# Performance work log

Measured on AMD Instinct MI355X. Metric: run time of the kernel, lower is better.

Reference implementation:

```python
import jax, jax.numpy as jnp
import numpy as np

B, N, D_IN, D = 4, 256, 128, 256
T = 3
EPS = 1e-5


def _layernorm(x, g, b):
    mu = x.mean(axis=-1, keepdims=True)
    var = x.var(axis=-1, keepdims=True)
    return (x - mu) * jax.lax.rsqrt(var + EPS) * g + b


def setup_inputs() -> dict:
    key = jax.random.key(0)
    ks = jax.random.split(key, 16)
    s = lambda k, shape, fan_in: jax.random.normal(k, shape, jnp.float32) / np.sqrt(fan_in)
    return {
        "inputs": jax.random.normal(ks[0], (B, N, D_IN), jnp.float32),
        "v_t": jax.random.normal(ks[1], (B, N, D), jnp.float32),
        "i_t": jnp.zeros((B, N, N), jnp.float32),
        # proj_inputs
        "Wp": s(ks[2], (D_IN, D), D_IN), "bp": jnp.zeros((D,), jnp.float32),
        # MLPAdjacency
        "Wx": s(ks[3], (D, D), D), "bx": jnp.zeros((D,), jnp.float32),
        "wi": s(ks[4], (D,), 1), "bi": jnp.zeros((D,), jnp.float32),
        "ws": s(ks[5], (D,), D), "bs": jnp.zeros((1,), jnp.float32),
        # LayerNorms
        "g_pre": jnp.ones((3 * D,), jnp.float32), "be_pre": jnp.zeros((3 * D,), jnp.float32),
        "g_n": jnp.ones((D,), jnp.float32), "be_n": jnp.zeros((D,), jnp.float32),
        # DeepSet(3D -> D -> D), equivariant layers: h@Wg + mean(h)@Wl + b
        "W1g": s(ks[6], (3 * D, D), 3 * D), "W1l": s(ks[7], (3 * D, D), 3 * D),
        "b1": jnp.zeros((D,), jnp.float32),
        "W2g": s(ks[8], (D, D), D), "W2l": s(ks[9], (D, D), D),
        "b2": jnp.zeros((D,), jnp.float32),
    }


def reference(inputs, v_t, i_t, Wp, bp, Wx, bx, wi, bi, ws, bs,
              g_pre, be_pre, g_n, be_n, W1g, W1l, b1, W2g, W2l, b2):
    x_in = inputs @ Wp + bp  # [b,n,d]
    n_t, inc = v_t, i_t
    preds = []
    for _ in range(T):
        # MLPAdjacency: [b,n,n,d] broadcast sum -> relu -> linear -> sigmoid
        xp = n_t @ Wx + bx
        s = jax.nn.relu(xp[:, None, :, :] + xp[:, :, None, :]
                        + inc[..., None] * wi + bi)
        inc = jax.nn.sigmoid(jnp.einsum('bend,d->ben', s, ws) + bs[0])  # [b,n,n]
        # aggregation
        upd = jnp.einsum('ben,bed->bnd', inc, n_t)
        # DeepSet over normalized concat, residual + LayerNorm
        h = _layernorm(jnp.concatenate([x_in, n_t, upd], axis=-1), g_pre, be_pre)
        m = h.mean(axis=1, keepdims=True)
        h1 = jax.nn.relu(h @ W1g + m @ W1l + b1)
        m1 = h1.mean(axis=1, keepdims=True)
        h2 = h1 @ W2g + m1 @ W2l + b2
        n_t = _layernorm(n_t + h2, g_n, be_n)
        preds.append(inc)
    return (jnp.stack(preds, axis=0), n_t, inc)
```

## Files before the change

kernel.cpp:

```cpp
#include <hip/hip_runtime.h>
#include <cstddef>

#define LN_EPS 1e-5f

__device__ inline float4 ld4(const float* p) { return *reinterpret_cast<const float4*>(p); }
__device__ inline void st4(float* p, float4 v) { *reinterpret_cast<float4*>(p) = v; }

__device__ __forceinline__ void gemm_dev(float* lds, const float* __restrict__ A,
                                         const float* __restrict__ W,
                                         const float* __restrict__ bias,
                                         float* __restrict__ dst,
                                         int K, int chunk, int row0, int col0, int k0) {
  float* At = lds;
  float* Ws = lds + 1088;
  const int tid = threadIdx.x;
  const int tx = tid & 15, ty = tid >> 4;
  float acc[4][4] = {{0.f}};
  const int arow = tid >> 2;
  const int ak4 = (tid & 3) * 4;
  const int wk = tid >> 4;
  const int wc4 = (tid & 15) * 4;
  float4 av = ld4(&A[(size_t)(row0 + arow) * K + k0 + ak4]);
  float4 wv = ld4(&W[(size_t)(k0 + wk) * 256 + col0 + wc4]);
  for (int ks = 0; ks < chunk; ks += 16) {
    __syncthreads();
    At[(ak4 + 0) * 68 + arow] = av.x;
    At[(ak4 + 1) * 68 + arow] = av.y;
    At[(ak4 + 2) * 68 + arow] = av.z;
    At[(ak4 + 3) * 68 + arow] = av.w;
    st4(&Ws[wk * 68 + wc4], wv);
    __syncthreads();
    if (ks + 16 < chunk) {
      av = ld4(&A[(size_t)(row0 + arow) * K + k0 + ks + 16 + ak4]);
      wv = ld4(&W[(size_t)(k0 + ks + 16 + wk) * 256 + col0 + wc4]);
    }
#pragma unroll
    for (int kk = 0; kk < 16; ++kk) {
      float4 a = ld4(&At[kk * 68 + ty * 4]);
      float4 w = ld4(&Ws[kk * 68 + tx * 4]);
      acc[0][0] = fmaf(a.x, w.x, acc[0][0]); acc[0][1] = fmaf(a.x, w.y, acc[0][1]);
      acc[0][2] = fmaf(a.x, w.z, acc[0][2]); acc[0][3] = fmaf(a.x, w.w, acc[0][3]);
      acc[1][0] = fmaf(a.y, w.x, acc[1][0]); acc[1][1] = fmaf(a.y, w.y, acc[1][1]);
      acc[1][2] = fmaf(a.y, w.z, acc[1][2]); acc[1][3] = fmaf(a.y, w.w, acc[1][3]);
      acc[2][0] = fmaf(a.z, w.x, acc[2][0]); acc[2][1] = fmaf(a.z, w.y, acc[2][1]);
      acc[2][2] = fmaf(a.z, w.z, acc[2][2]); acc[2][3] = fmaf(a.z, w.w, acc[2][3]);
      acc[3][0] = fmaf(a.w, w.x, acc[3][0]); acc[3][1] = fmaf(a.w, w.y, acc[3][1]);
      acc[3][2] = fmaf(a.w, w.z, acc[3][2]); acc[3][3] = fmaf(a.w, w.w, acc[3][3]);
    }
  }
  if (bias) {
    float4 b4 = ld4(&bias[col0 + tx * 4]);
#pragma unroll
    for (int i = 0; i < 4; ++i) {
      float4 o;
      o.x = acc[i][0] + b4.x; o.y = acc[i][1] + b4.y;
      o.z = acc[i][2] + b4.z; o.w = acc[i][3] + b4.w;
      st4(&dst[(size_t)(row0 + ty * 4 + i) * 256 + col0 + tx * 4], o);
    }
  } else {
#pragma unroll
    for (int i = 0; i < 4; ++i) {
      float4 o = {acc[i][0], acc[i][1], acc[i][2], acc[i][3]};
      st4(&dst[(size_t)(row0 + ty * 4 + i) * 256 + col0 + tx * 4], o);
    }
  }
}

__device__ __forceinline__ void gemm_h1(float* lds, const float* __restrict__ part,
                                        const float* __restrict__ mt1p,
                                        const float* __restrict__ W,
                                        float* __restrict__ dst,
                                        int gb, int row0, int col0, int k0) {
  float* At = lds;
  float* Ws = lds + 1088;
  float* mt1s = lds + 2176;
  const int tid = threadIdx.x;
  const int tx = tid & 15, ty = tid >> 4;
  if (tid < 64) {
    float s = 0.f;
#pragma unroll
    for (int k2 = 0; k2 < 12; ++k2) s += mt1p[((size_t)(k2 * 4 + gb) << 8) + k0 + tid];
    mt1s[tid] = s;
  }
  float acc[4][4] = {{0.f}};
  const int arow = tid >> 2;
  const int ak4 = (tid & 3) * 4;
  const int wk = tid >> 4;
  const int wc4 = (tid & 15) * 4;
  size_t ao = (size_t)(row0 + arow) * 256 + k0 + ak4;
  float4 p0 = ld4(&part[ao]);
  float4 p1 = ld4(&part[ao + 262144]);
  float4 p2 = ld4(&part[ao + 524288]);
  float4 p3 = ld4(&part[ao + 786432]);
  float4 wv = ld4(&W[(size_t)(k0 + wk) * 256 + col0 + wc4]);
  for (int ks = 0; ks < 64; ks += 16) {
    __syncthreads();
    float4 m = ld4(&mt1s[ks + ak4]);
    float4 av;
    av.x = fmaxf(p0.x + p1.x + p2.x + p3.x + m.x, 0.f);
    av.y = fmaxf(p0.y + p1.y + p2.y + p3.y + m.y, 0.f);
    av.z = fmaxf(p0.z + p1.z + p2.z + p3.z + m.z, 0.f);
    av.w = fmaxf(p0.w + p1.w + p2.w + p3.w + m.w, 0.f);
    At[(ak4 + 0) * 68 + arow] = av.x;
    At[(ak4 + 1) * 68 + arow] = av.y;
    At[(ak4 + 2) * 68 + arow] = av.z;
    At[(ak4 + 3) * 68 + arow] = av.w;
    st4(&Ws[wk * 68 + wc4], wv);
    __syncthreads();
    if (ks + 16 < 64) {
      size_t an = (size_t)(row0 + arow) * 256 + k0 + ks + 16 + ak4;
      p0 = ld4(&part[an]);
      p1 = ld4(&part[an + 262144]);
      p2 = ld4(&part[an + 524288]);
      p3 = ld4(&part[an + 786432]);
      wv = ld4(&W[(size_t)(k0 + ks + 16 + wk) * 256 + col0 + wc4]);
    }
#pragma unroll
    for (int kk = 0; kk < 16; ++kk) {
      float4 a = ld4(&At[kk * 68 + ty * 4]);
      float4 w = ld4(&Ws[kk * 68 + tx * 4]);
      acc[0][0] = fmaf(a.x, w.x, acc[0][0]); acc[0][1] = fmaf(a.x, w.y, acc[0][1]);
      acc[0][2] = fmaf(a.x, w.z, acc[0][2]); acc[0][3] = fmaf(a.x, w.w, acc[0][3]);
      acc[1][0] = fmaf(a.y, w.x, acc[1][0]); acc[1][1] = fmaf(a.y, w.y, acc[1][1]);
      acc[1][2] = fmaf(a.y, w.z, acc[1][2]); acc[1][3] = fmaf(a.y, w.w, acc[1][3]);
      acc[2][0] = fmaf(a.z, w.x, acc[2][0]); acc[2][1] = fmaf(a.z, w.y, acc[2][1]);
      acc[2][2] = fmaf(a.z, w.z, acc[2][2]); acc[2][3] = fmaf(a.z, w.w, acc[2][3]);
      acc[3][0] = fmaf(a.w, w.x, acc[3][0]); acc[3][1] = fmaf(a.w, w.y, acc[3][1]);
      acc[3][2] = fmaf(a.w, w.z, acc[3][2]); acc[3][3] = fmaf(a.w, w.w, acc[3][3]);
    }
  }
#pragma unroll
  for (int i = 0; i < 4; ++i) {
    float4 o = {acc[i][0], acc[i][1], acc[i][2], acc[i][3]};
    st4(&dst[(size_t)(row0 + ty * 4 + i) * 256 + col0 + tx * 4], o);
  }
}

__device__ __forceinline__ void gemmt_dev(float* lds, const float* __restrict__ pred,
                                          const float* __restrict__ nt,
                                          float* __restrict__ pp,
                                          int gb, int n0, int col0, int k0) {
  float* At = lds;
  float* Ws = lds + 1088;
  const int tid = threadIdx.x;
  const int tx = tid & 15, ty = tid >> 4;
  const float* Ab = pred + ((size_t)gb << 16);
  const float* Bb = nt + ((size_t)gb << 16);
  float acc[4][4] = {{0.f}};
  const int ee = tid >> 4;
  const int q4 = (tid & 15) * 4;
  float4 av = ld4(&Ab[((size_t)(k0 + ee) << 8) + n0 + q4]);
  float4 wv = ld4(&Bb[((size_t)(k0 + ee) << 8) + col0 + q4]);
  for (int ks = 0; ks < 64; ks += 16) {
    __syncthreads();
    st4(&At[ee * 68 + q4], av);
    st4(&Ws[ee * 68 + q4], wv);
    __syncthreads();
    if (ks + 16 < 64) {
      av = ld4(&Ab[((size_t)(k0 + ks + 16 + ee) << 8) + n0 + q4]);
      wv = ld4(&Bb[((size_t)(k0 + ks + 16 + ee) << 8) + col0 + q4]);
    }
#pragma unroll
    for (int kk = 0; kk < 16; ++kk) {
      float4 a = ld4(&At[kk * 68 + ty * 4]);
      float4 w = ld4(&Ws[kk * 68 + tx * 4]);
      acc[0][0] = fmaf(a.x, w.x, acc[0][0]); acc[0][1] = fmaf(a.x, w.y, acc[0][1]);
      acc[0][2] = fmaf(a.x, w.z, acc[0][2]); acc[0][3] = fmaf(a.x, w.w, acc[0][3]);
      acc[1][0] = fmaf(a.y, w.x, acc[1][0]); acc[1][1] = fmaf(a.y, w.y, acc[1][1]);
      acc[1][2] = fmaf(a.y, w.z, acc[1][2]); acc[1][3] = fmaf(a.y, w.w, acc[1][3]);
      acc[2][0] = fmaf(a.z, w.x, acc[2][0]); acc[2][1] = fmaf(a.z, w.y, acc[2][1]);
      acc[2][2] = fmaf(a.z, w.z, acc[2][2]); acc[2][3] = fmaf(a.z, w.w, acc[2][3]);
      acc[3][0] = fmaf(a.w, w.x, acc[3][0]); acc[3][1] = fmaf(a.w, w.y, acc[3][1]);
      acc[3][2] = fmaf(a.w, w.z, acc[3][2]); acc[3][3] = fmaf(a.w, w.w, acc[3][3]);
    }
  }
#pragma unroll
  for (int i = 0; i < 4; ++i) {
    float4 o = {acc[i][0], acc[i][1], acc[i][2], acc[i][3]};
    st4(&pp[(((size_t)gb << 8) + n0 + ty * 4 + i) * 256 + col0 + tx * 4], o);
  }
}

__device__ __forceinline__ void wred2(float& s, float& q) {
#pragma unroll
  for (int off = 32; off; off >>= 1) {
    s += __shfl_xor(s, off);
    q += __shfl_xor(q, off);
  }
}

__device__ __forceinline__ void mtk_dev(float* lds, const float* __restrict__ X,
                                        const float* __restrict__ Wl,
                                        const float* __restrict__ bias,
                                        float* __restrict__ mtp, int gb, int ks, int Kd) {
  float* sm = lds;
  float* m64 = lds + 256;
  const int tid = threadIdx.x;
  const int col = tid & 63, q = tid >> 6;
  const float* xb = X + (size_t)(gb * 256 + q * 64) * Kd + ks * 64 + col;
  float s = 0.f;
#pragma unroll 8
  for (int r = 0; r < 64; ++r) s += xb[(size_t)r * Kd];
  sm[tid] = s;
  __syncthreads();
  if (tid < 64) m64[tid] = (sm[tid] + sm[tid + 64] + sm[tid + 128] + sm[tid + 192]) * (1.f / 256.f);
  __syncthreads();
  const int c = tid;
  float acc = (ks == 0) ? bias[c] : 0.f;
  const float* wp = Wl + (size_t)ks * 64 * 256 + c;
#pragma unroll 8
  for (int k = 0; k < 64; ++k) acc = fmaf(m64[k], wp[(size_t)k * 256], acc);
  mtp[((size_t)(ks * 4 + gb) << 8) + c] = acc;
}

__device__ __forceinline__ void mtk_h1(float* lds, const float* __restrict__ part,
                                       const float* __restrict__ mt1p,
                                       const float* __restrict__ Wl,
                                       const float* __restrict__ bias,
                                       float* __restrict__ mtp, int gb, int ks) {
  float* sm = lds;
  float* m64 = lds + 256;
  const int tid = threadIdx.x;
  const int col = tid & 63, q = tid >> 6;
  float mt1v = 0.f;
#pragma unroll
  for (int k2 = 0; k2 < 12; ++k2) mt1v += mt1p[((size_t)(k2 * 4 + gb) << 8) + ks * 64 + col];
  const float* pb = part + (size_t)(gb * 256 + q * 64) * 256 + ks * 64 + col;
  float s = 0.f;
#pragma unroll 4
  for (int r = 0; r < 64; ++r) {
    size_t o = (size_t)r * 256;
    float v = pb[o] + pb[o + 262144] + pb[o + 524288] + pb[o + 786432] + mt1v;
    s += fmaxf(v, 0.f);
  }
  sm[tid] = s;
  __syncthreads();
  if (tid < 64) m64[tid] = (sm[tid] + sm[tid + 64] + sm[tid + 128] + sm[tid + 192]) * (1.f / 256.f);
  __syncthreads();
  const int c = tid;
  float acc = (ks == 0) ? bias[c] : 0.f;
  const float* wp = Wl + (size_t)ks * 64 * 256 + c;
#pragma unroll 8
  for (int k = 0; k < 64; ++k) acc = fmaf(m64[k], wp[(size_t)k * 256], acc);
  mtp[((size_t)(ks * 4 + gb) << 8) + c] = acc;
}


__global__ __launch_bounds__(256) void k_gemm(const float* __restrict__ A,
                                              const float* __restrict__ W,
                                              const float* __restrict__ bias,
                                              float* __restrict__ dst,
                                              int K, int chunk) {
  __shared__ float lds[2176];
  float* base = bias ? dst : dst + (size_t)blockIdx.z * 262144;
  gemm_dev(lds, A, W, bias, base, K, chunk,
           blockIdx.x * 64, blockIdx.y * 64, blockIdx.z * chunk);
}

__global__ __launch_bounds__(256) void k_gemm0(const float* __restrict__ v_t,
                                               const float* __restrict__ Wx,
                                               float* __restrict__ part,
                                               const float* __restrict__ inputs,
                                               const float* __restrict__ Wp,
                                               const float* __restrict__ bp,
                                               float* __restrict__ x_in) {
  __shared__ float lds[2176];
  const int b = blockIdx.x;
  if (b < 256) {
    int mt = b & 15, ntile = (b >> 4) & 3, kz = b >> 6;
    gemm_dev(lds, v_t, Wx, nullptr, part + (size_t)kz * 262144, 256, 64,
             mt * 64, ntile * 64, kz * 64);
  } else {
    int idx = b - 256;
    int mt = idx & 15, ntile = idx >> 4;
    gemm_dev(lds, inputs, Wp, bp, x_in, 128, 128, mt * 64, ntile * 64, 0);
  }
}

__global__ __launch_bounds__(256) void k_adj(const float* __restrict__ part,
                                             const float* __restrict__ incold,
                                             const float* __restrict__ wi,
                                             const float* __restrict__ bi,
                                             const float* __restrict__ bx,
                                             const float* __restrict__ wsv,
                                             const float* __restrict__ bs,
                                             float* __restrict__ pred,
                                             float* __restrict__ pred2) {
  __shared__ float lds[8448];
  float* tn = lds;
  float* te = lds + 32 * 132;
  const int n0 = blockIdx.x * 32, e0 = blockIdx.y * 32, gb = blockIdx.z;
  const int tid = threadIdx.x;
  const size_t rb = (size_t)gb * 256;
  const int tx = tid & 15, ty = tid >> 4;
  float incv[2][2], acc[2][2];
#pragma unroll
  for (int j = 0; j < 2; ++j)
#pragma unroll
    for (int i = 0; i < 2; ++i) {
      incv[j][i] = incold[((rb + e0 + ty + 16 * j) << 8) + n0 + tx + 16 * i];
      acc[j][i] = 0.f;
    }
  for (int dh = 0; dh < 256; dh += 128) {
    if (dh) __syncthreads();
#pragma unroll
    for (int s = 0; s < 4; ++s) {
      int idx = tid + s * 256;
      int row = idx >> 5;
      int d = dh + (idx & 31) * 4;
      float4 bxv = ld4(&bx[d]);
      {
        size_t o = ((rb + n0 + row) << 8) + d;
        float4 p0 = ld4(&part[o]);
        float4 p1 = ld4(&part[o + 262144]);
        float4 p2 = ld4(&part[o + 524288]);
        float4 p3 = ld4(&part[o + 786432]);
        float4 v;
        v.x = p0.x + p1.x + p2.x + p3.x + bxv.x;
        v.y = p0.y + p1.y + p2.y + p3.y + bxv.y;
        v.z = p0.z + p1.z + p2.z + p3.z + bxv.z;
        v.w = p0.w + p1.w + p2.w + p3.w + bxv.w;
        st4(&tn[row * 132 + (d - dh)], v);
      }
      {
        size_t o = ((rb + e0 + row) << 8) + d;
        float4 p0 = ld4(&part[o]);
        float4 p1 = ld4(&part[o + 262144]);
        float4 p2 = ld4(&part[o + 524288]);
        float4 p3 = ld4(&part[o + 786432]);
        float4 bv = ld4(&bi[d]);
        float4 v;
        v.x = p0.x + p1.x + p2.x + p3.x + bxv.x + bv.x;
        v.y = p0.y + p1.y + p2.y + p3.y + bxv.y + bv.y;
        v.z = p0.z + p1.z + p2.z + p3.z + bxv.z + bv.z;
        v.w = p0.w + p1.w + p2.w + p3.w + bxv.w + bv.w;
        st4(&te[row * 132 + (d - dh)], v);
      }
    }
    __syncthreads();
#pragma unroll 4
    for (int dl = 0; dl < 128; dl += 4) {
      float4 wiq = ld4(&wi[dh + dl]);
      float4 wsq = ld4(&wsv[dh + dl]);
      float4 xn0 = ld4(&tn[tx * 132 + dl]);
      float4 xn1 = ld4(&tn[(tx + 16) * 132 + dl]);
      float4 xe0 = ld4(&te[ty * 132 + dl]);
      float4 xe1 = ld4(&te[(ty + 16) * 132 + dl]);
#pragma unroll
      for (int j = 0; j < 2; ++j) {
        float4 xe = j ? xe1 : xe0;
#pragma unroll
        for (int i = 0; i < 2; ++i) {
          float4 xn = i ? xn1 : xn0;
          float u;
          u = fmaf(incv[j][i], wiq.x, xn.x + xe.x); u = fmaxf(u, 0.f); acc[j][i] = fmaf(u, wsq.x, acc[j][i]);
          u = fmaf(incv[j][i], wiq.y, xn.y + xe.y); u = fmaxf(u, 0.f); acc[j][i] = fmaf(u, wsq.y, acc[j][i]);
          u = fmaf(incv[j][i], wiq.z, xn.z + xe.z); u = fmaxf(u, 0.f); acc[j][i] = fmaf(u, wsq.z, acc[j][i]);
          u = fmaf(incv[j][i], wiq.w, xn.w + xe.w); u = fmaxf(u, 0.f); acc[j][i] = fmaf(u, wsq.w, acc[j][i]);
        }
      }
    }
  }
  const float b0 = bs[0];
#pragma unroll
  for (int j = 0; j < 2; ++j)
#pragma unroll
    for (int i = 0; i < 2; ++i) {
      float s = acc[j][i] + b0;
      float v = 1.f / (1.f + __expf(-s));
      size_t o = ((rb + e0 + ty + 16 * j) << 8) + n0 + tx + 16 * i;
      pred[o] = v;
      if (pred2) pred2[o] = v;
    }
}

__global__ __launch_bounds__(256) void k_gemmt(const float* __restrict__ pred,
                                               const float* __restrict__ nt,
                                               float* __restrict__ part) {
  __shared__ float lds[2176];
  const int gb = blockIdx.z >> 2, kc = blockIdx.z & 3;
  gemmt_dev(lds, pred, nt, part + (size_t)kc * 262144,
            gb, blockIdx.x * 64, blockIdx.y * 64, kc * 64);
}

__global__ __launch_bounds__(256) void k_ln768(const float* __restrict__ part,
                                               const float* __restrict__ x_in,
                                               const float* __restrict__ nt,
                                               const float* __restrict__ g,
                                               const float* __restrict__ be,
                                               float* __restrict__ h) {
  const int row = blockIdx.x * 4 + (threadIdx.x >> 6);
  const int lane = threadIdx.x & 63;
  const int c4 = lane * 4;
  const size_t ro = (size_t)row * 256 + c4;
  float4 u = ld4(&part[ro]);
  float4 u1 = ld4(&part[ro + 262144]);
  float4 u2 = ld4(&part[ro + 524288]);
  float4 u3 = ld4(&part[ro + 786432]);
  u.x += u1.x + u2.x + u3.x;
  u.y += u1.y + u2.y + u3.y;
  u.z += u1.z + u2.z + u3.z;
  u.w += u1.w + u2.w + u3.w;
  float4 xi = ld4(&x_in[ro]);
  float4 nv = ld4(&nt[ro]);
  float s = xi.x + xi.y + xi.z + xi.w + nv.x + nv.y + nv.z + nv.w + u.x + u.y + u.z + u.w;
  float sq = xi.x * xi.x + xi.y * xi.y + xi.z * xi.z + xi.w * xi.w
           + nv.x * nv.x + nv.y * nv.y + nv.z * nv.z + nv.w * nv.w
           + u.x * u.x + u.y * u.y + u.z * u.z + u.w * u.w;
  wred2(s, sq);
  float mu = s * (1.f / 768.f);
  float rs = rsqrtf(sq * (1.f / 768.f) - mu * mu + LN_EPS);
  float* hr = h + (size_t)row * 768;
  {
    float4 g4 = ld4(&g[c4]), b4 = ld4(&be[c4]), o;
    o.x = (xi.x - mu) * rs * g4.x + b4.x;
    o.y = (xi.y - mu) * rs * g4.y + b4.y;
    o.z = (xi.z - mu) * rs * g4.z + b4.z;
    o.w = (xi.w - mu) * rs * g4.w + b4.w;
    st4(&hr[c4], o);
  }
  {
    float4 g4 = ld4(&g[256 + c4]), b4 = ld4(&be[256 + c4]), o;
    o.x = (nv.x - mu) * rs * g4.x + b4.x;
    o.y = (nv.y - mu) * rs * g4.y + b4.y;
    o.z = (nv.z - mu) * rs * g4.z + b4.z;
    o.w = (nv.w - mu) * rs * g4.w + b4.w;
    st4(&hr[256 + c4], o);
  }
  {
    float4 g4 = ld4(&g[512 + c4]), b4 = ld4(&be[512 + c4]), o;
    o.x = (u.x - mu) * rs * g4.x + b4.x;
    o.y = (u.y - mu) * rs * g4.y + b4.y;
    o.z = (u.z - mu) * rs * g4.z + b4.z;
    o.w = (u.w - mu) * rs * g4.w + b4.w;
    st4(&hr[512 + c4], o);
  }
}

__global__ __launch_bounds__(256) void k_g768mtk(const float* __restrict__ h,
                                                 const float* __restrict__ W1g,
                                                 const float* __restrict__ W1l,
                                                 const float* __restrict__ b1,
                                                 float* __restrict__ part,
                                                 float* __restrict__ mt1p) {
  __shared__ float lds[2176];
  const int b = blockIdx.x;
  if (b < 256) {
    int mt = b & 15, ntile = (b >> 4) & 3, kz = b >> 6;
    gemm_dev(lds, h, W1g, nullptr, part + (size_t)kz * 262144, 768, 192,
             mt * 64, ntile * 64, kz * 192);
  } else {
    int idx = b - 256;
    mtk_dev(lds, h, W1l, b1, mt1p, idx & 3, idx >> 2, 768);
  }
}

__global__ __launch_bounds__(256) void k_gh1mtk2(const float* __restrict__ part,
                                                 const float* __restrict__ mt1p,
                                                 const float* __restrict__ W2g,
                                                 const float* __restrict__ W2l,
                                                 const float* __restrict__ b2,
                                                 float* __restrict__ part2,
                                                 float* __restrict__ mt2p) {
  __shared__ float lds[2240];
  const int b = blockIdx.x;
  if (b < 256) {
    int mt = b & 15, ntile = (b >> 4) & 3, kz = b >> 6;
    gemm_h1(lds, part, mt1p, W2g, part2 + (size_t)kz * 262144,
            mt >> 2, mt * 64, ntile * 64, kz * 64);
  } else {
    int idx = b - 256;
    mtk_h1(lds, part, mt1p, W2l, b2, mt2p, idx & 3, idx >> 2);
  }
}

__global__ __launch_bounds__(256) void k_ln256(const float* __restrict__ part2,
                                               const float* __restrict__ nt,
                                               const float* __restrict__ mt2p,
                                               const float* __restrict__ g,
                                               const float* __restrict__ be,
                                               float* __restrict__ dst) {
  const int row = blockIdx.x * 4 + (threadIdx.x >> 6);
  const int lane = threadIdx.x & 63;
  const int c4 = lane * 4;
  const int gb = row >> 8;
  const size_t ro = (size_t)row * 256 + c4;
  float4 p0 = ld4(&part2[ro]);
  float4 p1 = ld4(&part2[ro + 262144]);
  float4 p2 = ld4(&part2[ro + 524288]);
  float4 p3 = ld4(&part2[ro + 786432]);
  float4 m4 = {0.f, 0.f, 0.f, 0.f};
#pragma unroll
  for (int k2 = 0; k2 < 4; ++k2) {
    float4 mv = ld4(&mt2p[((size_t)(k2 * 4 + gb) << 8) + c4]);
    m4.x += mv.x; m4.y += mv.y; m4.z += mv.z; m4.w += mv.w;
  }
  float4 nv = ld4(&nt[ro]);
  float4 x;
  x.x = nv.x + p0.x + p1.x + p2.x + p3.x + m4.x;
  x.y = nv.y + p0.y + p1.y + p2.y + p3.y + m4.y;
  x.z = nv.z + p0.z + p1.z + p2.z + p3.z + m4.z;
  x.w = nv.w + p0.w + p1.w + p2.w + p3.w + m4.w;
  float s = x.x + x.y + x.z + x.w;
  float sq = x.x * x.x + x.y * x.y + x.z * x.z + x.w * x.w;
  wred2(s, sq);
  float mu = s * (1.f / 256.f);
  float rs = rsqrtf(sq * (1.f / 256.f) - mu * mu + LN_EPS);
  float4 g4 = ld4(&g[c4]), b4 = ld4(&be[c4]), o;
  o.x = (x.x - mu) * rs * g4.x + b4.x;
  o.y = (x.y - mu) * rs * g4.y + b4.y;
  o.z = (x.z - mu) * rs * g4.z + b4.z;
  o.w = (x.w - mu) * rs * g4.w + b4.w;
  st4(&dst[ro], o);
}

extern "C" void kernel_launch(void* const* d_in, const int* in_sizes, int n_in,
                              void* d_out, int out_size, void* d_ws, size_t ws_size,
                              hipStream_t stream) {
  (void)in_sizes; (void)n_in; (void)out_size; (void)ws_size;
  const float* inputs = (const float*)d_in[0];
  const float* v_t    = (const float*)d_in[1];
  const float* i_t    = (const float*)d_in[2];
  const float* Wp     = (const float*)d_in[3];
  const float* bp     = (const float*)d_in[4];
  const float* Wx     = (const float*)d_in[5];
  const float* bx     = (const float*)d_in[6];
  const float* wi     = (const float*)d_in[7];
  const float* bi     = (const float*)d_in[8];
  const float* ws     = (const float*)d_in[9];
  const float* bs     = (const float*)d_in[10];
  const float* g_pre  = (const float*)d_in[11];
  const float* be_pre = (const float*)d_in[12];
  const float* g_n    = (const float*)d_in[13];
  const float* be_n   = (const float*)d_in[14];
  const float* W1g    = (const float*)d_in[15];
  const float* W1l    = (const float*)d_in[16];
  const float* b1     = (const float*)d_in[17];
  const float* W2g    = (const float*)d_in[18];
  const float* W2l    = (const float*)d_in[19];
  const float* b2     = (const float*)d_in[20];
  float* out = (float*)d_out;
  float* wsf = (float*)d_ws;
  float* x_in  = wsf;
  float* ntA   = wsf + 262144;
  float* ntB   = wsf + 524288;
  float* h     = wsf + 786432;
  float* part2 = wsf + 786432;
  float* part  = wsf + 1835008;
  float* mt1p  = wsf + 2883584;
  float* mt2p  = wsf + 2895872;

  for (int t = 0; t < 3; ++t) {
    const float* ntCur = (t == 0) ? v_t : ((t == 1) ? ntA : ntB);
    float* dstNt = (t == 2) ? (out + 786432) : ((t == 0) ? ntA : ntB);
    const float* incold = (t == 0) ? i_t : (out + (size_t)(t - 1) * 262144);
    float* pred = out + (size_t)t * 262144;
    float* pred2 = (t == 2) ? (out + 1048576) : nullptr;

    if (t == 0) {
      k_gemm0<<<320, 256, 0, stream>>>(v_t, Wx, part, inputs, Wp, bp, x_in);
    } else {
      k_gemm<<<dim3(16, 4, 4), 256, 0, stream>>>(ntCur, Wx, nullptr, part, 256, 64);
    }
    k_adj<<<dim3(8, 8, 4), 256, 0, stream>>>(part, incold, wi, bi, bx, ws, bs, pred, pred2);
    k_gemmt<<<dim3(4, 4, 16), 256, 0, stream>>>(pred, ntCur, part);
    k_ln768<<<256, 256, 0, stream>>>(part, x_in, ntCur, g_pre, be_pre, h);
    k_g768mtk<<<304, 256, 0, stream>>>(h, W1g, W1l, b1, part, mt1p);
    k_gh1mtk2<<<272, 256, 0, stream>>>(part, mt1p, W2g, W2l, b2, part2, mt2p);
    k_ln256<<<256, 256, 0, stream>>>(part2, ntCur, mt2p, g_n, be_n, dstNt);
  }
}
```

Baseline: 198.6 us.

## Switch tiled SIMT GEMMs to packed fp16 dot2 with fp32 accumulation

New measurement: 193.4 us (median of 2 runs). 2.6% less time.

```diff
diff --git a/kernel.cpp b/kernel.cpp
--- a/kernel.cpp
+++ b/kernel.cpp
@@ -6,46 +6,73 @@
 __device__ inline float4 ld4(const float* p) { return *reinterpret_cast<const float4*>(p); }
 __device__ inline void st4(float* p, float4 v) { *reinterpret_cast<float4*>(p) = v; }
 
-__device__ __forceinline__ void gemm_dev(float* lds, const float* __restrict__ A,
-                                         const float* __restrict__ W,
-                                         const float* __restrict__ bias,
-                                         float* __restrict__ dst,
-                                         int K, int chunk, int row0, int col0, int k0) {
-  float* At = lds;
-  float* Ws = lds + 1088;
+typedef _Float16 h2_t __attribute__((ext_vector_type(2)));
+
+__device__ __forceinline__ unsigned pack2(float x, float y) {
+  h2_t h;
+  h.x = (_Float16)x;
+  h.y = (_Float16)y;
+  return __builtin_bit_cast(unsigned, h);
+}
+
+__device__ __forceinline__ float dot2(unsigned a, unsigned b, float c) {
+  h2_t ah = __builtin_bit_cast(h2_t, a);
+  h2_t bh = __builtin_bit_cast(h2_t, b);
+#if __has_builtin(__builtin_amdgcn_fdot2)
+  return __builtin_amdgcn_fdot2(ah, bh, c, false);
+#else
+  return fmaf((float)ah.x, (float)bh.x, fmaf((float)ah.y, (float)bh.y, c));
+#endif
+}
+
+__device__ __forceinline__ void gemm16(unsigned* ldsU, const float* __restrict__ A,
+                                       const float* __restrict__ W,
+                                       const float* __restrict__ bias,
+                                       float* __restrict__ dst,
+                                       int K, int chunk, int row0, int col0, int k0) {
+  unsigned* AtU = ldsU;
+  unsigned* WsU = ldsU + 544;
   const int tid = threadIdx.x;
   const int tx = tid & 15, ty = tid >> 4;
+  const int arow = tid >> 2, ak4 = (tid & 3) * 4;
+  const int wkk2 = tid >> 4, wc4 = (tid & 15) * 4;
   float acc[4][4] = {{0.f}};
-  const int arow = tid >> 2;
-  const int ak4 = (tid & 3) * 4;
-  const int wk = tid >> 4;
-  const int wc4 = (tid & 15) * 4;
   float4 av = ld4(&A[(size_t)(row0 + arow) * K + k0 + ak4]);
-  float4 wv = ld4(&W[(size_t)(k0 + wk) * 256 + col0 + wc4]);
+  float4 w0, w1;
+  if (tid < 128) {
+    w0 = ld4(&W[(size_t)(k0 + 2 * wkk2) * 256 + col0 + wc4]);
+    w1 = ld4(&W[(size_t)(k0 + 2 * wkk2 + 1) * 256 + col0 + wc4]);
+  }
   for (int ks = 0; ks < chunk; ks += 16) {
     __syncthreads();
-    At[(ak4 + 0) * 68 + arow] = av.x;
-    At[(ak4 + 1) * 68 + arow] = av.y;
-    At[(ak4 + 2) * 68 + arow] = av.z;
-    At[(ak4 + 3) * 68 + arow] = av.w;
-    st4(&Ws[wk * 68 + wc4], wv);
+    AtU[(ak4 >> 1) * 68 + arow] = pack2(av.x, av.y);
+    AtU[((ak4 >> 1) + 1) * 68 + arow] = pack2(av.z, av.w);
+    if (tid < 128) {
+      WsU[wkk2 * 68 + wc4 + 0] = pack2(w0.x, w1.x);
+      WsU[wkk2 * 68 + wc4 + 1] = pack2(w0.y, w1.y);
+      WsU[wkk2 * 68 + wc4 + 2] = pack2(w0.z, w1.z);
+      WsU[wkk2 * 68 + wc4 + 3] = pack2(w0.w, w1.w);
+    }
     __syncthreads();
     if (ks + 16 < chunk) {
       av = ld4(&A[(size_t)(row0 + arow) * K + k0 + ks + 16 + ak4]);
-      wv = ld4(&W[(size_t)(k0 + ks + 16 + wk) * 256 + col0 + wc4]);
-    }
-#pragma unroll
-    for (int kk = 0; kk < 16; ++kk) {
-      float4 a = ld4(&At[kk * 68 + ty * 4]);
-      float4 w = ld4(&Ws[kk * 68 + tx * 4]);
-      acc[0][0] = fmaf(a.x, w.x, acc[0][0]); acc[0][1] = fmaf(a.x, w.y, acc[0][1]);
-      acc[0][2] = fmaf(a.x, w.z, acc[0][2]); acc[0][3] = fmaf(a.x, w.w, acc[0][3]);
-      acc[1][0] = fmaf(a.y, w.x, acc[1][0]); acc[1][1] = fmaf(a.y, w.y, acc[1][1]);
-      acc[1][2] = fmaf(a.y, w.z, acc[1][2]); acc[1][3] = fmaf(a.y, w.w, acc[1][3]);
-      acc[2][0] = fmaf(a.z, w.x, acc[2][0]); acc[2][1] = fmaf(a.z, w.y, acc[2][1]);
-      acc[2][2] = fmaf(a.z, w.z, acc[2][2]); acc[2][3] = fmaf(a.z, w.w, acc[2][3]);
-      acc[3][0] = fmaf(a.w, w.x, acc[3][0]); acc[3][1] = fmaf(a.w, w.y, acc[3][1]);
-      acc[3][2] = fmaf(a.w, w.z, acc[3][2]); acc[3][3] = fmaf(a.w, w.w, acc[3][3]);
+      if (tid < 128) {
+        w0 = ld4(&W[(size_t)(k0 + ks + 16 + 2 * wkk2) * 256 + col0 + wc4]);
+        w1 = ld4(&W[(size_t)(k0 + ks + 16 + 2 * wkk2 + 1) * 256 + col0 + wc4]);
+      }
+    }
+#pragma unroll
+    for (int kk2 = 0; kk2 < 8; ++kk2) {
+      uint4 a4 = *reinterpret_cast<const uint4*>(&AtU[kk2 * 68 + ty * 4]);
+      uint4 w4 = *reinterpret_cast<const uint4*>(&WsU[kk2 * 68 + tx * 4]);
+      acc[0][0] = dot2(a4.x, w4.x, acc[0][0]); acc[0][1] = dot2(a4.x, w4.y, acc[0][1]);
+      acc[0][2] = dot2(a4.x, w4.z, acc[0][2]); acc[0][3] = dot2(a4.x, w4.w, acc[0][3]);
+      acc[1][0] = dot2(a4.y, w4.x, acc[1][0]); acc[1][1] = dot2(a4.y, w4.y, acc[1][1]);
+      acc[1][2] = dot2(a4.y, w4.z, acc[1][2]); acc[1][3] = dot2(a4.y, w4.w, acc[1][3]);
+      acc[2][0] = dot2(a4.z, w4.x, acc[2][0]); acc[2][1] = dot2(a4.z, w4.y, acc[2][1]);
+      acc[2][2] = dot2(a4.z, w4.z, acc[2][2]); acc[2][3] = dot2(a4.z, w4.w, acc[2][3]);
+      acc[3][0] = dot2(a4.w, w4.x, acc[3][0]); acc[3][1] = dot2(a4.w, w4.y, acc[3][1]);
+      acc[3][2] = dot2(a4.w, w4.z, acc[3][2]); acc[3][3] = dot2(a4.w, w4.w, acc[3][3]);
     }
   }
   if (bias) {
@@ -66,16 +93,68 @@
   }
 }
 
-__device__ __forceinline__ void gemm_h1(float* lds, const float* __restrict__ part,
-                                        const float* __restrict__ mt1p,
-                                        const float* __restrict__ W,
-                                        float* __restrict__ dst,
-                                        int gb, int row0, int col0, int k0) {
-  float* At = lds;
-  float* Ws = lds + 1088;
-  float* mt1s = lds + 2176;
+__device__ __forceinline__ void gemmt16(unsigned* ldsU, const float* __restrict__ pred,
+                                        const float* __restrict__ nt,
+                                        float* __restrict__ pp,
+                                        int gb, int n0, int col0, int k0) {
+  unsigned* AtU = ldsU;
+  unsigned* WsU = ldsU + 544;
   const int tid = threadIdx.x;
   const int tx = tid & 15, ty = tid >> 4;
+  const float* Ab = pred + ((size_t)gb << 16);
+  const float* Bb = nt + ((size_t)gb << 16);
+  const int t7 = tid & 127;
+  const int ee2 = t7 >> 4, cg4 = (t7 & 15) * 4;
+  const int base = (tid < 128) ? n0 : col0;
+  const float* src = (tid < 128) ? Ab : Bb;
+  unsigned* dstU = (tid < 128) ? AtU : WsU;
+  float acc[4][4] = {{0.f}};
+  float4 r0 = ld4(&src[((size_t)(k0 + 2 * ee2) << 8) + base + cg4]);
+  float4 r1 = ld4(&src[((size_t)(k0 + 2 * ee2 + 1) << 8) + base + cg4]);
+  for (int ks = 0; ks < 64; ks += 16) {
+    __syncthreads();
+    dstU[ee2 * 68 + cg4 + 0] = pack2(r0.x, r1.x);
+    dstU[ee2 * 68 + cg4 + 1] = pack2(r0.y, r1.y);
+    dstU[ee2 * 68 + cg4 + 2] = pack2(r0.z, r1.z);
+    dstU[ee2 * 68 + cg4 + 3] = pack2(r0.w, r1.w);
+    __syncthreads();
+    if (ks + 16 < 64) {
+      r0 = ld4(&src[((size_t)(k0 + ks + 16 + 2 * ee2) << 8) + base + cg4]);
+      r1 = ld4(&src[((size_t)(k0 + ks + 16 + 2 * ee2 + 1) << 8) + base + cg4]);
+    }
+#pragma unroll
+    for (int kk2 = 0; kk2 < 8; ++kk2) {
+      uint4 a4 = *reinterpret_cast<const uint4*>(&AtU[kk2 * 68 + ty * 4]);
+      uint4 w4 = *reinterpret_cast<const uint4*>(&WsU[kk2 * 68 + tx * 4]);
+      acc[0][0] = dot2(a4.x, w4.x, acc[0][0]); acc[0][1] = dot2(a4.x, w4.y, acc[0][1]);
+      acc[0][2] = dot2(a4.x, w4.z, acc[0][2]); acc[0][3] = dot2(a4.x, w4.w, acc[0][3]);
+      acc[1][0] = dot2(a4.y, w4.x, acc[1][0]); acc[1][1] = dot2(a4.y, w4.y, acc[1][1]);
+      acc[1][2] = dot2(a4.y, w4.z, acc[1][2]); acc[1][3] = dot2(a4.y, w4.w, acc[1][3]);
+      acc[2][0] = dot2(a4.z, w4.x, acc[2][0]); acc[2][1] = dot2(a4.z, w4.y, acc[2][1]);
+      acc[2][2] = dot2(a4.z, w4.z, acc[2][2]); acc[2][3] = dot2(a4.z, w4.w, acc[2][3]);
+      acc[3][0] = dot2(a4.w, w4.x, acc[3][0]); acc[3][1] = dot2(a4.w, w4.y, acc[3][1]);
+      acc[3][2] = dot2(a4.w, w4.z, acc[3][2]); acc[3][3] = dot2(a4.w, w4.w, acc[3][3]);
+    }
+  }
+#pragma unroll
+  for (int i = 0; i < 4; ++i) {
+    float4 o = {acc[i][0], acc[i][1], acc[i][2], acc[i][3]};
+    st4(&pp[(((size_t)gb << 8) + n0 + ty * 4 + i) * 256 + col0 + tx * 4], o);
+  }
+}
+
+__device__ __forceinline__ void gemm_h116(unsigned* ldsU, const float* __restrict__ part,
+                                          const float* __restrict__ mt1p,
+                                          const float* __restrict__ W,
+                                          float* __restrict__ dst,
+                                          int gb, int row0, int col0, int k0) {
+  unsigned* AtU = ldsU;
+  unsigned* WsU = ldsU + 544;
+  float* mt1s = reinterpret_cast<float*>(ldsU + 1088);
+  const int tid = threadIdx.x;
+  const int tx = tid & 15, ty = tid >> 4;
+  const int arow = tid >> 2, ak4 = (tid & 3) * 4;
+  const int wkk2 = tid >> 4, wc4 = (tid & 15) * 4;
   if (tid < 64) {
     float s = 0.f;
 #pragma unroll
@@ -83,29 +162,31 @@
     mt1s[tid] = s;
   }
   float acc[4][4] = {{0.f}};
-  const int arow = tid >> 2;
-  const int ak4 = (tid & 3) * 4;
-  const int wk = tid >> 4;
-  const int wc4 = (tid & 15) * 4;
   size_t ao = (size_t)(row0 + arow) * 256 + k0 + ak4;
   float4 p0 = ld4(&part[ao]);
   float4 p1 = ld4(&part[ao + 262144]);
   float4 p2 = ld4(&part[ao + 524288]);
   float4 p3 = ld4(&part[ao + 786432]);
-  float4 wv = ld4(&W[(size_t)(k0 + wk) * 256 + col0 + wc4]);
+  float4 w0, w1;
+  if (tid < 128) {
+    w0 = ld4(&W[(size_t)(k0 + 2 * wkk2) * 256 + col0 + wc4]);
+    w1 = ld4(&W[(size_t)(k0 + 2 * wkk2 + 1) * 256 + col0 + wc4]);
+  }
   for (int ks = 0; ks < 64; ks += 16) {
     __syncthreads();
     float4 m = ld4(&mt1s[ks + ak4]);
-    float4 av;
-    av.x = fmaxf(p0.x + p1.x + p2.x + p3.x + m.x, 0.f);
-    av.y = fmaxf(p0.y + p1.y + p2.y + p3.y + m.y, 0.f);
-    av.z = fmaxf(p0.z + p1.z + p2.z + p3.z + m.z, 0.f);
-    av.w = fmaxf(p0.w + p1.w + p2.w + p3.w + m.w, 0.f);
-    At[(ak4 + 0) * 68 + arow] = av.x;
-    At[(ak4 + 1) * 68 + arow] = av.y;
-    At[(ak4 + 2) * 68 + arow] = av.z;
-    At[(ak4 + 3) * 68 + arow] = av.w;
-    st4(&Ws[wk * 68 + wc4], wv);
+    float ax = fmaxf(p0.x + p1.x + p2.x + p3.x + m.x, 0.f);
+    float ay = fmaxf(p0.y + p1.y + p2.y + p3.y + m.y, 0.f);
+    float az = fmaxf(p0.z + p1.z + p2.z + p3.z + m.z, 0.f);
+    float aw = fmaxf(p0.w + p1.w + p2.w + p3.w + m.w, 0.f);
+    AtU[(ak4 >> 1) * 68 + arow] = pack2(ax, ay);
+    AtU[((ak4 >> 1) + 1) * 68 + arow] = pack2(az, aw);
+    if (tid < 128) {
+      WsU[wkk2 * 68 + wc4 + 0] = pack2(w0.x, w1.x);
+      WsU[wkk2 * 68 + wc4 + 1] = pack2(w0.y, w1.y);
+      WsU[wkk2 * 68 + wc4 + 2] = pack2(w0.z, w1.z);
+      WsU[wkk2 * 68 + wc4 + 3] = pack2(w0.w, w1.w);
+    }
     __syncthreads();
     if (ks + 16 < 64) {
       size_t an = (size_t)(row0 + arow) * 256 + k0 + ks + 16 + ak4;
@@ -113,71 +194,29 @@
       p1 = ld4(&part[an + 262144]);
       p2 = ld4(&part[an + 524288]);
       p3 = ld4(&part[an + 786432]);
-      wv = ld4(&W[(size_t)(k0 + ks + 16 + wk) * 256 + col0 + wc4]);
-    }
-#pragma unroll
-    for (int kk = 0; kk < 16; ++kk) {
-      float4 a = ld4(&At[kk * 68 + ty * 4]);
-      float4 w = ld4(&Ws[kk * 68 + tx * 4]);
-      acc[0][0] = fmaf(a.x, w.x, acc[0][0]); acc[0][1] = fmaf(a.x, w.y, acc[0][1]);
-      acc[0][2] = fmaf(a.x, w.z, acc[0][2]); acc[0][3] = fmaf(a.x, w.w, acc[0][3]);
-      acc[1][0] = fmaf(a.y, w.x, acc[1][0]); acc[1][1] = fmaf(a.y, w.y, acc[1][1]);
-      acc[1][2] = fmaf(a.y, w.z, acc[1][2]); acc[1][3] = fmaf(a.y, w.w, acc[1][3]);
-      acc[2][0] = fmaf(a.z, w.x, acc[2][0]); acc[2][1] = fmaf(a.z, w.y, acc[2][1]);
-      acc[2][2] = fmaf(a.z, w.z, acc[2][2]); acc[2][3] = fmaf(a.z, w.w, acc[2][3]);
-      acc[3][0] = fmaf(a.w, w.x, acc[3][0]); acc[3][1] = fmaf(a.w, w.y, acc[3][1]);
-      acc[3][2] = fmaf(a.w, w.z, acc[3][2]); acc[3][3] = fmaf(a.w, w.w, acc[3][3]);
+      if (tid < 128) {
+        w0 = ld4(&W[(size_t)(k0 + ks + 16 + 2 * wkk2) * 256 + col0 + wc4]);
+        w1 = ld4(&W[(size_t)(k0 + ks + 16 + 2 * wkk2 + 1) * 256 + col0 + wc4]);
+      }
+    }
+#pragma unroll
+    for (int kk2 = 0; kk2 < 8; ++kk2) {
+      uint4 a4 = *reinterpret_cast<const uint4*>(&AtU[kk2 * 68 + ty * 4]);
+      uint4 w4 = *reinterpret_cast<const uint4*>(&WsU[kk2 * 68 + tx * 4]);
+      acc[0][0] = dot2(a4.x, w4.x, acc[0][0]); acc[0][1] = dot2(a4.x, w4.y, acc[0][1]);
+      acc[0][2] = dot2(a4.x, w4.z, acc[0][2]); acc[0][3] = dot2(a4.x, w4.w, acc[0][3]);
+      acc[1][0] = dot2(a4.y, w4.x, acc[1][0]); acc[1][1] = dot2(a4.y, w4.y, acc[1][1]);
+      acc[1][2] = dot2(a4.y, w4.z, acc[1][2]); acc[1][3] = dot2(a4.y, w4.w, acc[1][3]);
+      acc[2][0] = dot2(a4.z, w4.x, acc[2][0]); acc[2][1] = dot2(a4.z, w4.y, acc[2][1]);
+      acc[2][2] = dot2(a4.z, w4.z, acc[2][2]); acc[2][3] = dot2(a4.z, w4.w, acc[2][3]);
+      acc[3][0] = dot2(a4.w, w4.x, acc[3][0]); acc[3][1] = dot2(a4.w, w4.y, acc[3][1]);
+      acc[3][2] = dot2(a4.w, w4.z, acc[3][2]); acc[3][3] = dot2(a4.w, w4.w, acc[3][3]);
     }
   }
 #pragma unroll
   for (int i = 0; i < 4; ++i) {
     float4 o = {acc[i][0], acc[i][1], acc[i][2], acc[i][3]};
     st4(&dst[(size_t)(row0 + ty * 4 + i) * 256 + col0 + tx * 4], o);
-  }
-}
-
-__device__ __forceinline__ void gemmt_dev(float* lds, const float* __restrict__ pred,
-                                          const float* __restrict__ nt,
-                                          float* __restrict__ pp,
-                                          int gb, int n0, int col0, int k0) {
-  float* At = lds;
-  float* Ws = lds + 1088;
-  const int tid = threadIdx.x;
-  const int tx = tid & 15, ty = tid >> 4;
-  const float* Ab = pred + ((size_t)gb << 16);
-  const float* Bb = nt + ((size_t)gb << 16);
-  float acc[4][4] = {{0.f}};
-  const int ee = tid >> 4;
-  const int q4 = (tid & 15) * 4;
-  float4 av = ld4(&Ab[((size_t)(k0 + ee) << 8) + n0 + q4]);
-  float4 wv = ld4(&Bb[((size_t)(k0 + ee) << 8) + col0 + q4]);
-  for (int ks = 0; ks < 64; ks += 16) {
-    __syncthreads();
-    st4(&At[ee * 68 + q4], av);
-    st4(&Ws[ee * 68 + q4], wv);
-    __syncthreads();
-    if (ks + 16 < 64) {
-      av = ld4(&Ab[((size_t)(k0 + ks + 16 + ee) << 8) + n0 + q4]);
-      wv = ld4(&Bb[((size_t)(k0 + ks + 16 + ee) << 8) + col0 + q4]);
-    }
-#pragma unroll
-    for (int kk = 0; kk < 16; ++kk) {
-      float4 a = ld4(&At[kk * 68 + ty * 4]);
-      float4 w = ld4(&Ws[kk * 68 + tx * 4]);
-      acc[0][0] = fmaf(a.x, w.x, acc[0][0]); acc[0][1] = fmaf(a.x, w.y, acc[0][1]);
-      acc[0][2] = fmaf(a.x, w.z, acc[0][2]); acc[0][3] = fmaf(a.x, w.w, acc[0][3]);
-      acc[1][0] = fmaf(a.y, w.x, acc[1][0]); acc[1][1] = fmaf(a.y, w.y, acc[1][1]);
-      acc[1][2] = fmaf(a.y, w.z, acc[1][2]); acc[1][3] = fmaf(a.y, w.w, acc[1][3]);
-      acc[2][0] = fmaf(a.z, w.x, acc[2][0]); acc[2][1] = fmaf(a.z, w.y, acc[2][1]);
-      acc[2][2] = fmaf(a.z, w.z, acc[2][2]); acc[2][3] = fmaf(a.z, w.w, acc[2][3]);
-      acc[3][0] = fmaf(a.w, w.x, acc[3][0]); acc[3][1] = fmaf(a.w, w.y, acc[3][1]);
-      acc[3][2] = fmaf(a.w, w.z, acc[3][2]); acc[3][3] = fmaf(a.w, w.w, acc[3][3]);
-    }
-  }
-#pragma unroll
-  for (int i = 0; i < 4; ++i) {
-    float4 o = {acc[i][0], acc[i][1], acc[i][2], acc[i][3]};
-    st4(&pp[(((size_t)gb << 8) + n0 + ty * 4 + i) * 256 + col0 + tx * 4], o);
   }
 }
 
@@ -251,10 +290,10 @@
                                               const float* __restrict__ bias,
                                               float* __restrict__ dst,
                                               int K, int chunk) {
-  __shared__ float lds[2176];
+  __shared__ unsigned ldsU[1088];
   float* base = bias ? dst : dst + (size_t)blockIdx.z * 262144;
-  gemm_dev(lds, A, W, bias, base, K, chunk,
-           blockIdx.x * 64, blockIdx.y * 64, blockIdx.z * chunk);
+  gemm16(ldsU, A, W, bias, base, K, chunk,
+         blockIdx.x * 64, blockIdx.y * 64, blockIdx.z * chunk);
 }
 
 __global__ __launch_bounds__(256) void k_gemm0(const float* __restrict__ v_t,
@@ -264,16 +303,16 @@
                                                const float* __restrict__ Wp,
                                                const float* __restrict__ bp,
                                                float* __restrict__ x_in) {
-  __shared__ float lds[2176];
+  __shared__ unsigned ldsU[1088];
   const int b = blockIdx.x;
   if (b < 256) {
     int mt = b & 15, ntile = (b >> 4) & 3, kz = b >> 6;
-    gemm_dev(lds, v_t, Wx, nullptr, part + (size_t)kz * 262144, 256, 64,
-             mt * 64, ntile * 64, kz * 64);
+    gemm16(ldsU, v_t, Wx, nullptr, part + (size_t)kz * 262144, 256, 64,
+           mt * 64, ntile * 64, kz * 64);
   } else {
     int idx = b - 256;
     int mt = idx & 15, ntile = idx >> 4;
-    gemm_dev(lds, inputs, Wp, bp, x_in, 128, 128, mt * 64, ntile * 64, 0);
+    gemm16(ldsU, inputs, Wp, bp, x_in, 128, 128, mt * 64, ntile * 64, 0);
   }
 }
 
@@ -377,10 +416,10 @@
 __global__ __launch_bounds__(256) void k_gemmt(const float* __restrict__ pred,
                                                const float* __restrict__ nt,
                                                float* __restrict__ part) {
-  __shared__ float lds[2176];
+  __shared__ unsigned ldsU[1088];
   const int gb = blockIdx.z >> 2, kc = blockIdx.z & 3;
-  gemmt_dev(lds, pred, nt, part + (size_t)kc * 262144,
-            gb, blockIdx.x * 64, blockIdx.y * 64, kc * 64);
+  gemmt16(ldsU, pred, nt, part + (size_t)kc * 262144,
+          gb, blockIdx.x * 64, blockIdx.y * 64, kc * 64);
 }
 
 __global__ __launch_bounds__(256) void k_ln768(const float* __restrict__ part,
@@ -443,15 +482,15 @@
                                                  const float* __restrict__ b1,
                                                  float* __restrict__ part,
                                                  float* __restrict__ mt1p) {
-  __shared__ float lds[2176];
+  __shared__ unsigned ldsU[1088];
   const int b = blockIdx.x;
   if (b < 256) {
     int mt = b & 15, ntile = (b >> 4) & 3, kz = b >> 6;
-    gemm_dev(lds, h, W1g, nullptr, part + (size_t)kz * 262144, 768, 192,
-             mt * 64, ntile * 64, kz * 192);
+    gemm16(ldsU, h, W1g, nullptr, part + (size_t)kz * 262144, 768, 192,
+           mt * 64, ntile * 64, kz * 192);
   } else {
     int idx = b - 256;
-    mtk_dev(lds, h, W1l, b1, mt1p, idx & 3, idx >> 2, 768);
+    mtk_dev(reinterpret_cast<float*>(ldsU), h, W1l, b1, mt1p, idx & 3, idx >> 2, 768);
   }
 }
 
@@ -462,15 +501,15 @@
                                                  const float* __restrict__ b2,
                                                  float* __restrict__ part2,
                                                  float* __restrict__ mt2p) {
-  __shared__ float lds[2240];
+  __shared__ unsigned ldsU[1152];
   const int b = blockIdx.x;
   if (b < 256) {
     int mt = b & 15, ntile = (b >> 4) & 3, kz = b >> 6;
-    gemm_h1(lds, part, mt1p, W2g, part2 + (size_t)kz * 262144,
-            mt >> 2, mt * 64, ntile * 64, kz * 64);
+    gemm_h116(ldsU, part, mt1p, W2g, part2 + (size_t)kz * 262144,
+              mt >> 2, mt * 64, ntile * 64, kz * 64);
   } else {
     int idx = b - 256;
-    mtk_h1(lds, part, mt1p, W2l, b2, mt2p, idx & 3, idx >> 2);
+    mtk_h1(reinterpret_cast<float*>(ldsU), part, mt1p, W2l, b2, mt2p, idx & 3, idx >> 2);
   }
 }
 
```
